# Performance work log

Measured on AMD Instinct MI355X. Metric: run time of the kernel, lower is better.

Reference implementation:

```python
import jax, jax.numpy as jnp
import numpy as np

C = 1024
H = 64
W = 64


def _conv1x1(x, Wt, b):
    # x: [1, Cin, H, W], Wt: [Cout, Cin] -> [1, Cout, H, W]
    return jnp.einsum('oc,bchw->bohw', Wt, x) + b[None, :, None, None]


def setup_inputs() -> dict:
    key = jax.random.key(0)
    ks = jax.random.split(key, 12)
    sc = 1.0 / np.sqrt(C)
    return {
        'x_f': jax.random.normal(ks[0], (1, C, H, W), jnp.float32),
        'x_m': jax.random.normal(ks[1], (1, C, H, W), jnp.float32),
        'x_l': jax.random.normal(ks[2], (1, C, H, W), jnp.float32),
        'Wq': jax.random.normal(ks[3], (C // 2, C), jnp.float32) * sc,
        'bq': jax.random.normal(ks[4], (C // 2,), jnp.float32) * sc,
        'Wk1': jax.random.normal(ks[5], (C // 2, C), jnp.float32) * sc,
        'bk1': jax.random.normal(ks[6], (C // 2,), jnp.float32) * sc,
        'Wk2': jax.random.normal(ks[7], (C // 2, C), jnp.float32) * sc,
        'bk2': jax.random.normal(ks[8], (C // 2,), jnp.float32) * sc,
        'Wv': jax.random.normal(ks[9], (C, C), jnp.float32) * sc,
        'bv': jax.random.normal(ks[10], (C,), jnp.float32) * sc,
        'gamma': jax.random.normal(ks[11], (1,), jnp.float32),
    }


def reference(x_f, x_m, x_l, Wq, bq, Wk1, bk1, Wk2, bk2, Wv, bv, gamma):
    c = x_f.shape[1]
    h, w = x_f.shape[2], x_f.shape[3]
    # torch .view(1, C, -1) on a [1, C/2, H, W] tensor: row-major reshape to [C, H*W/2]
    q = _conv1x1(x_m, Wq, bq).reshape(c, -1).T      # [HW/2, C]
    kf = _conv1x1(x_f, Wk1, bk1).reshape(c, -1)     # [C, HW/2]
    kl = _conv1x1(x_l, Wk2, bk2).reshape(c, -1)     # [C, HW/2]
    att_f = jax.nn.softmax(kf @ q, axis=-1)         # [C, C]
    att_l = jax.nn.softmax(kl @ q, axis=-1)         # [C, C]
    v = _conv1x1(x_m, Wv, bv).reshape(c, -1)        # [C, HW]
    out = att_f @ v + att_l @ v                     # [C, HW]
    out = out.reshape(1, c, h, w)
    return gamma * out + (x_l + x_f) / 2
```

## Files before the change

### kernel.cpp

```cpp
#include <hip/hip_runtime.h>
#include <math.h>


typedef __attribute__((ext_vector_type(8))) short    bf16x8;
typedef __attribute__((ext_vector_type(4))) float    f32x4;

__device__ __forceinline__ unsigned short f2bf(float x) {
    unsigned u = __float_as_uint(x);
    u += 0x7FFFu + ((u >> 16) & 1u);
    return (unsigned short)(u >> 16);
}
__device__ __forceinline__ float bf2f(unsigned short h) {
    return __uint_as_float(((unsigned)h) << 16);
}
__device__ __forceinline__ void split2(float x, unsigned short& h, unsigned short& l) {
    h = f2bf(x);
    l = f2bf(x - bf2f(h));
}

__device__ __forceinline__ size_t swz(int m, int k, int kpan) {
    return ((size_t)((m >> 4) * kpan + (k >> 5))) * 512
         + (size_t)((((k >> 3) & 3) * 16 + (m & 15)) * 8 + (k & 7));
}

__device__ __forceinline__ void gld16(const unsigned short* g, unsigned short* l) {
    __builtin_amdgcn_global_load_lds(
        (const __attribute__((address_space(1))) unsigned int*)g,
        (__attribute__((address_space(3))) unsigned int*)l,
        16, 0, 0);
}

__global__ __launch_bounds__(256) void weights_split_k(
    const float* __restrict__ Wq, const float* __restrict__ Wk1,
    const float* __restrict__ Wk2, const float* __restrict__ Wv,
    unsigned short* __restrict__ Wqh, unsigned short* __restrict__ Wql,
    unsigned short* __restrict__ Wk1h, unsigned short* __restrict__ Wk1l,
    unsigned short* __restrict__ Wk2h, unsigned short* __restrict__ Wk2l,
    unsigned short* __restrict__ Wvh, unsigned short* __restrict__ Wvl)
{
    const int gi = blockIdx.x;
    const float* src; unsigned short *H, *L; int base;
    if (gi < 512)       { src = Wq;  H = Wqh;  L = Wql;  base = gi; }
    else if (gi < 1024) { src = Wk1; H = Wk1h; L = Wk1l; base = gi - 512; }
    else if (gi < 1536) { src = Wk2; H = Wk2h; L = Wk2l; base = gi - 1024; }
    else                { src = Wv;  H = Wvh;  L = Wvl;  base = gi - 1536; }
    const size_t i = (size_t)base * 1024 + threadIdx.x * 4;
    const int m = (int)(i >> 10);
    const int k = (int)(i & 1023);
    const float4 v = *(const float4*)(src + i);
    ushort4 h, l;
    split2(v.x, h.x, l.x); split2(v.y, h.y, l.y);
    split2(v.z, h.z, l.z); split2(v.w, h.w, l.w);
    const size_t o = swz(m, k, 32);
    *(ushort4*)(H + o) = h;
    *(ushort4*)(L + o) = l;
}

__global__ __launch_bounds__(256) void transpose3_k(
    const float* __restrict__ x0, const float* __restrict__ x1,
    const float* __restrict__ x2,
    unsigned short* __restrict__ t0h, unsigned short* __restrict__ t0l,
    unsigned short* __restrict__ t1h, unsigned short* __restrict__ t1l,
    unsigned short* __restrict__ t2h, unsigned short* __restrict__ t2l)
{
    const float* X; unsigned short *Th, *Tl;
    if (blockIdx.z == 0)      { X = x0; Th = t0h; Tl = t0l; }
    else if (blockIdx.z == 1) { X = x1; Th = t1h; Tl = t1l; }
    else                      { X = x2; Th = t2h; Tl = t2l; }

    __shared__ float t[32 * 33];
    const int tid = threadIdx.x;
    const int c0 = blockIdx.y * 32;
    const int p0 = blockIdx.x * 32;

    const int cl = tid >> 3;
    const int p4 = (tid & 7) * 4;
    const float4 v = *(const float4*)(X + (size_t)(c0 + cl) * 4096 + p0 + p4);
    t[(p4 + 0) * 33 + cl] = v.x;
    t[(p4 + 1) * 33 + cl] = v.y;
    t[(p4 + 2) * 33 + cl] = v.z;
    t[(p4 + 3) * 33 + cl] = v.w;
    __syncthreads();

    const int pl = tid >> 3;
    const int c4 = (tid & 7) * 4;
    ushort4 h, l;
    split2(t[pl * 33 + c4 + 0], h.x, l.x);
    split2(t[pl * 33 + c4 + 1], h.y, l.y);
    split2(t[pl * 33 + c4 + 2], h.z, l.z);
    split2(t[pl * 33 + c4 + 3], h.w, l.w);
    const size_t o = (size_t)(p0 + pl) * 1024 + c0 + c4;
    *(ushort4*)(Th + o) = h;
    *(ushort4*)(Tl + o) = l;
}

__global__ __launch_bounds__(256) void transpose1_k(
    const float* __restrict__ X,
    unsigned short* __restrict__ Th, unsigned short* __restrict__ Tl)
{
    __shared__ float t[32 * 33];
    const int tid = threadIdx.x;
    const int c0 = blockIdx.y * 32;
    const int p0 = blockIdx.x * 32;

    const int cl = tid >> 3;
    const int p4 = (tid & 7) * 4;
    const float4 v = *(const float4*)(X + (size_t)(c0 + cl) * 4096 + p0 + p4);
    t[(p4 + 0) * 33 + cl] = v.x;
    t[(p4 + 1) * 33 + cl] = v.y;
    t[(p4 + 2) * 33 + cl] = v.z;
    t[(p4 + 3) * 33 + cl] = v.w;
    __syncthreads();

    const int pl = tid >> 3;
    const int c4 = (tid & 7) * 4;
    ushort4 h, l;
    split2(t[pl * 33 + c4 + 0], h.x, l.x);
    split2(t[pl * 33 + c4 + 1], h.y, l.y);
    split2(t[pl * 33 + c4 + 2], h.z, l.z);
    split2(t[pl * 33 + c4 + 3], h.w, l.w);
    const size_t o = (size_t)(p0 + pl) * 1024 + c0 + c4;
    *(ushort4*)(Th + o) = h;
    *(ushort4*)(Tl + o) = l;
}

template<int TERMS>
__device__ __forceinline__ void gemm_core(
    const unsigned short* __restrict__ Ah, const unsigned short* __restrict__ Al,
    const unsigned short* __restrict__ Bh, const unsigned short* __restrict__ Bl,
    int ldkB, int kpanA, int kbeg, int kend, int m0, int n0,
    unsigned short* Bs_h, unsigned short* Bs_l,
    f32x4 (&acc)[4][4])
{
    const int tid  = threadIdx.x;
    const int lane = tid & 63;
    const int wv   = tid >> 6;
    const int wm   = (wv >> 1) * 64;
    const int wn   = (wv & 1) * 64;
    const int lr   = lane & 15;
    const int quad = lane >> 4;

    const unsigned short* gsrc = (wv < 2) ? Bh : Bl;
    unsigned short* ldst = (wv < 2) ? Bs_h : Bs_l;
    const int tt0  = (wv & 1) * 4;
    const int lrow = lane >> 2;
    const int gseg = ((lane & 3) - ((lane >> 3) & 3)) & 3;
    const unsigned short* gp[4];
#pragma unroll
    for (int u = 0; u < 4; ++u)
        gp[u] = gsrc + (size_t)(n0 + (tt0 + u) * 16 + lrow) * ldkB + kbeg + gseg * 8;

    const int pk0 = kbeg >> 5;
    const unsigned short* ap[4];
    const unsigned short* apl[4];
#pragma unroll
    for (int i = 0; i < 4; ++i) {
        const size_t off = ((size_t)(((m0 + wm) >> 4) + i) * kpanA + pk0) * 512
                         + (size_t)lane * 8;
        ap[i] = Ah + off;
        apl[i] = (TERMS == 3) ? (Al + off) : nullptr;
    }

    const int rdseg = (quad + (lr >> 1)) & 3;

#pragma unroll
    for (int u = 0; u < 4; ++u) {
        gld16(gp[u], ldst + (tt0 + u) * 512);
        gp[u] += 32;
    }

    int buf = 0;
    for (int k0 = kbeg; k0 < kend; k0 += 32) {
        __syncthreads();

        bf16x8 afh[4], afl[4];
#pragma unroll
        for (int i = 0; i < 4; ++i) {
            afh[i] = *(const bf16x8*)ap[i];  ap[i] += 512;
            if (TERMS == 3) { afl[i] = *(const bf16x8*)apl[i]; apl[i] += 512; }
        }
        if (k0 + 32 < kend) {
#pragma unroll
            for (int u = 0; u < 4; ++u) {
                gld16(gp[u], ldst + (buf ^ 1) * 4096 + (tt0 + u) * 512);
                gp[u] += 32;
            }
        }
        bf16x8 bfh[4], bfl[4];
#pragma unroll
        for (int j = 0; j < 4; ++j) {
            const int rb = buf * 4096 + (wn + j * 16 + lr) * 32 + rdseg * 8;
            bfh[j] = *(const bf16x8*)(Bs_h + rb);
            bfl[j] = *(const bf16x8*)(Bs_l + rb);
        }
#pragma unroll
        for (int i = 0; i < 4; ++i)
#pragma unroll
            for (int j = 0; j < 4; ++j) {
                acc[i][j] = __builtin_amdgcn_mfma_f32_16x16x32_bf16(afh[i], bfh[j], acc[i][j], 0, 0, 0);
                acc[i][j] = __builtin_amdgcn_mfma_f32_16x16x32_bf16(afh[i], bfl[j], acc[i][j], 0, 0, 0);
                if (TERMS == 3)
                    acc[i][j] = __builtin_amdgcn_mfma_f32_16x16x32_bf16(afl[i], bfh[j], acc[i][j], 0, 0, 0);
            }
        buf ^= 1;
    }
}

#define GEMM_PROLOGUE()                                                 \
    __shared__ __align__(16) unsigned short Bs_h[2 * 128 * 32];         \
    __shared__ __align__(16) unsigned short Bs_l[2 * 128 * 32];         \
    f32x4 acc[4][4];                                                    \
    _Pragma("unroll") for (int i = 0; i < 4; ++i)                       \
    _Pragma("unroll") for (int j = 0; j < 4; ++j)                       \
    _Pragma("unroll") for (int r = 0; r < 4; ++r) acc[i][j][r] = 0.f;   \
    const int lane = threadIdx.x & 63;                                  \
    const int wv   = threadIdx.x >> 6;                                  \
    const int wm   = (wv >> 1) * 64;                                    \
    const int wn   = (wv & 1) * 64;                                     \
    const int lr   = lane & 15;                                         \
    const int quad = lane >> 4;                                         \
    (void)lane; (void)wv;

__global__ __launch_bounds__(256) void conv_all_k(
    const unsigned short* __restrict__ Wqh, const unsigned short* __restrict__ Wql,
    const unsigned short* __restrict__ Wk1h, const unsigned short* __restrict__ Wk1l,
    const unsigned short* __restrict__ Wk2h, const unsigned short* __restrict__ Wk2l,
    const unsigned short* __restrict__ Wvh, const unsigned short* __restrict__ Wvl,
    const unsigned short* __restrict__ xmTh, const unsigned short* __restrict__ xmTl,
    const unsigned short* __restrict__ xfTh, const unsigned short* __restrict__ xfTl,
    const unsigned short* __restrict__ xlTh, const unsigned short* __restrict__ xlTl,
    const float* __restrict__ bq, const float* __restrict__ bk1,
    const float* __restrict__ bk2, const float* __restrict__ bv,
    unsigned short* __restrict__ Qh, unsigned short* __restrict__ Ql,
    unsigned short* __restrict__ Kfh, unsigned short* __restrict__ Kfl,
    unsigned short* __restrict__ Klh, unsigned short* __restrict__ Kll,
    float* __restrict__ V)
{
    GEMM_PROLOGUE();
    const int mt = blockIdx.y;
    const unsigned short *Ah, *Al, *Bh, *Bl;
    const float* bias;
    unsigned short *Ch = nullptr, *Cl = nullptr;
    float* Cv = nullptr;
    int mloc, mode;
    if (mt < 4) {
        Ah = Wqh;  Al = Wql;  Bh = xmTh; Bl = xmTl; bias = bq;
        Ch = Qh;   Cl = Ql;   mloc = mt * 128;        mode = 0;
    } else if (mt < 8) {
        Ah = Wk1h; Al = Wk1l; Bh = xfTh; Bl = xfTl; bias = bk1;
        Ch = Kfh;  Cl = Kfl;  mloc = (mt - 4) * 128;  mode = 1;
    } else if (mt < 12) {
        Ah = Wk2h; Al = Wk2l; Bh = xlTh; Bl = xlTl; bias = bk2;
        Ch = Klh;  Cl = Kll;  mloc = (mt - 8) * 128;  mode = 1;
    } else {
        Ah = Wvh;  Al = Wvl;  Bh = xmTh; Bl = xmTl; bias = bv;
        Cv = V;    mloc = (mt - 12) * 128;            mode = 2;
    }
    const int n0 = blockIdx.x * 128;

    gemm_core<3>(Ah, Al, Bh, Bl, 1024, 32, 0, 1024, mloc, n0, Bs_h, Bs_l, acc);

#pragma unroll
    for (int i = 0; i < 4; ++i) {
        const int mb = mloc + wm + i * 16 + quad * 4;
#pragma unroll
        for (int j = 0; j < 4; ++j) {
            const int nn = n0 + wn + j * 16 + lr;
#pragma unroll
            for (int r = 0; r < 4; ++r) {
                const float v = acc[i][j][r] + bias[mb + r];
                if (mode == 2) {
                    Cv[(size_t)(mb + r) * 4096 + nn] = v;
                } else if (mode == 0) {
                    unsigned short h, l;
                    split2(v, h, l);
                    const size_t idx = (size_t)(mb + r) * 4096 + nn;
                    Ch[idx] = h;
                    Cl[idx] = l;
                } else {
                    const int m2 = ((mb + r) << 1) | (nn >> 11);
                    const int k2 = nn & 2047;
                    const size_t o = swz(m2, k2, 64);
                    unsigned short h, l;
                    split2(v, h, l);
                    Ch[o] = h;
                    Cl[o] = l;
                }
            }
        }
    }
}

__global__ __launch_bounds__(256) void logits_fused_k(
    const unsigned short* __restrict__ Kfh, const unsigned short* __restrict__ Kfl,
    const unsigned short* __restrict__ Klh, const unsigned short* __restrict__ Kll,
    const unsigned short* __restrict__ Qh, const unsigned short* __restrict__ Ql,
    float* __restrict__ Sfp, float* __restrict__ Slp)
{
    GEMM_PROLOGUE();
    const int which = blockIdx.z >> 2;
    const int slice = blockIdx.z & 3;
    const unsigned short* Ah = which ? Klh : Kfh;
    const unsigned short* Al = which ? Kll : Kfl;
    float* out = (which ? Slp : Sfp) + (size_t)slice * 1024 * 1024;
    const int m0 = blockIdx.y * 128;
    const int n0 = blockIdx.x * 128;

    gemm_core<3>(Ah, Al, Qh, Ql, 2048, 64, slice * 512, slice * 512 + 512, m0, n0,
                 Bs_h, Bs_l, acc);

#pragma unroll
    for (int i = 0; i < 4; ++i) {
        const int mb = m0 + wm + i * 16 + quad * 4;
#pragma unroll
        for (int j = 0; j < 4; ++j) {
            const int nn = n0 + wn + j * 16 + lr;
#pragma unroll
            for (int r = 0; r < 4; ++r)
                out[(size_t)(mb + r) * 1024 + nn] = acc[i][j][r];
        }
    }
}

__global__ __launch_bounds__(256) void gemm_final_k(
    const unsigned short* __restrict__ Amh,
    const unsigned short* __restrict__ VTh, const unsigned short* __restrict__ VTl,
    float* __restrict__ out,
    const float* __restrict__ xf, const float* __restrict__ xl,
    const float* __restrict__ gamma)
{
    GEMM_PROLOGUE();
    const int m0 = blockIdx.y * 128;
    const int n0 = blockIdx.x * 128;

    gemm_core<2>(Amh, nullptr, VTh, VTl, 1024, 32, 0, 1024, m0, n0, Bs_h, Bs_l, acc);

    const float g = gamma[0];
#pragma unroll
    for (int i = 0; i < 4; ++i) {
        const int mb = m0 + wm + i * 16 + quad * 4;
#pragma unroll
        for (int j = 0; j < 4; ++j) {
            const int nn = n0 + wn + j * 16 + lr;
#pragma unroll
            for (int r = 0; r < 4; ++r) {
                const size_t idx = (size_t)(mb + r) * 4096 + nn;
                out[idx] = g * acc[i][j][r] + 0.5f * (xf[idx] + xl[idx]);
            }
        }
    }
}

__global__ __launch_bounds__(256) void softmax_add4_k(
    const float* __restrict__ Sfp, const float* __restrict__ Slp,
    unsigned short* __restrict__ Ah)
{
    const int row = blockIdx.x;
    const int tid = threadIdx.x;
    __shared__ float red[8];
    const size_t base = (size_t)row * 1024 + tid * 4;
    const size_t SL = (size_t)1024 * 1024;

    float4 vf = *(const float4*)(Sfp + base);
    float4 vl = *(const float4*)(Slp + base);
#pragma unroll
    for (int s = 1; s < 4; ++s) {
        const float4 a = *(const float4*)(Sfp + s * SL + base);
        const float4 b = *(const float4*)(Slp + s * SL + base);
        vf.x += a.x; vf.y += a.y; vf.z += a.z; vf.w += a.w;
        vl.x += b.x; vl.y += b.y; vl.z += b.z; vl.w += b.w;
    }

    float mf = fmaxf(fmaxf(vf.x, vf.y), fmaxf(vf.z, vf.w));
    float ml = fmaxf(fmaxf(vl.x, vl.y), fmaxf(vl.z, vl.w));
#pragma unroll
    for (int off = 32; off; off >>= 1) {
        mf = fmaxf(mf, __shfl_down(mf, off, 64));
        ml = fmaxf(ml, __shfl_down(ml, off, 64));
    }
    const int wave = tid >> 6;
    if ((tid & 63) == 0) { red[wave] = mf; red[4 + wave] = ml; }
    __syncthreads();
    mf = fmaxf(fmaxf(red[0], red[1]), fmaxf(red[2], red[3]));
    ml = fmaxf(fmaxf(red[4], red[5]), fmaxf(red[6], red[7]));
    __syncthreads();

    const float4 ef = make_float4(expf(vf.x - mf), expf(vf.y - mf),
                                  expf(vf.z - mf), expf(vf.w - mf));
    const float4 el = make_float4(expf(vl.x - ml), expf(vl.y - ml),
                                  expf(vl.z - ml), expf(vl.w - ml));
    float sf = ef.x + ef.y + ef.z + ef.w;
    float sl = el.x + el.y + el.z + el.w;
#pragma unroll
    for (int off = 32; off; off >>= 1) {
        sf += __shfl_down(sf, off, 64);
        sl += __shfl_down(sl, off, 64);
    }
    if ((tid & 63) == 0) { red[wave] = sf; red[4 + wave] = sl; }
    __syncthreads();
    sf = red[0] + red[1] + red[2] + red[3];
    sl = red[4] + red[5] + red[6] + red[7];

    const float rf = 1.f / sf, rl = 1.f / sl;
    ushort4 h;
    h.x = f2bf(ef.x * rf + el.x * rl);
    h.y = f2bf(ef.y * rf + el.y * rl);
    h.z = f2bf(ef.z * rf + el.z * rl);
    h.w = f2bf(ef.w * rf + el.w * rl);
    const size_t o = swz(row, tid * 4, 32);
    *(ushort4*)(Ah + o) = h;
}

__global__ void noop_k(float* p) { if (threadIdx.x == 1024) p[0] = 0.f; }

extern "C" void kernel_launch(void* const* d_in, const int* in_sizes, int n_in,
                              void* d_out, int out_size, void* d_ws, size_t ws_size,
                              hipStream_t stream) {
    (void)in_sizes; (void)n_in; (void)out_size;
    const float* xf  = (const float*)d_in[0];
    const float* xm  = (const float*)d_in[1];
    const float* xl  = (const float*)d_in[2];
    const float* Wq  = (const float*)d_in[3];
    const float* bq  = (const float*)d_in[4];
    const float* Wk1 = (const float*)d_in[5];
    const float* bk1 = (const float*)d_in[6];
    const float* Wk2 = (const float*)d_in[7];
    const float* bk2 = (const float*)d_in[8];
    const float* Wv  = (const float*)d_in[9];
    const float* bv  = (const float*)d_in[10];
    const float* gamma = (const float*)d_in[11];
    float* out = (float*)d_out;

    const size_t MB = 1024 * 1024;
    if (ws_size < 98 * MB) {
        noop_k<<<dim3(1), dim3(64), 0, stream>>>((float*)d_ws);
        return;
    }

    char* p = (char*)d_ws;
    unsigned short* xmT_h = (unsigned short*)(p + 0 * MB);
    unsigned short* xmT_l = (unsigned short*)(p + 8 * MB);
    unsigned short* xfT_h = (unsigned short*)(p + 16 * MB);
    unsigned short* xfT_l = (unsigned short*)(p + 24 * MB);
    unsigned short* xlT_h = (unsigned short*)(p + 32 * MB);
    unsigned short* xlT_l = (unsigned short*)(p + 40 * MB);
    unsigned short* Wq_h  = (unsigned short*)(p + 48 * MB);
    unsigned short* Wq_l  = (unsigned short*)(p + 49 * MB);
    unsigned short* Wk1_h = (unsigned short*)(p + 50 * MB);
    unsigned short* Wk1_l = (unsigned short*)(p + 51 * MB);
    unsigned short* Wk2_h = (unsigned short*)(p + 52 * MB);
    unsigned short* Wk2_l = (unsigned short*)(p + 53 * MB);
    unsigned short* Wv_h  = (unsigned short*)(p + 54 * MB);
    unsigned short* Wv_l  = (unsigned short*)(p + 56 * MB);
    unsigned short* Q_h   = (unsigned short*)(p + 58 * MB);
    unsigned short* Q_l   = (unsigned short*)(p + 62 * MB);
    unsigned short* Kf_h  = (unsigned short*)(p + 66 * MB);
    unsigned short* Kf_l  = (unsigned short*)(p + 70 * MB);
    unsigned short* Kl_h  = (unsigned short*)(p + 74 * MB);
    unsigned short* Kl_l  = (unsigned short*)(p + 78 * MB);
    float*          V     = (float*)(p + 82 * MB);
    float*          Sfp  = (float*)(p + 16 * MB);
    float*          Slp  = (float*)(p + 32 * MB);
    unsigned short* VT_h = xmT_h;
    unsigned short* VT_l = xmT_l;
    unsigned short* Am_h = (unsigned short*)(p + 74 * MB);

    const dim3 blk(256);
    transpose3_k<<<dim3(128, 32, 3), blk, 0, stream>>>(
        xm, xf, xl, xmT_h, xmT_l, xfT_h, xfT_l, xlT_h, xlT_l);
    weights_split_k<<<dim3(2560), blk, 0, stream>>>(
        Wq, Wk1, Wk2, Wv, Wq_h, Wq_l, Wk1_h, Wk1_l, Wk2_h, Wk2_l, Wv_h, Wv_l);
    conv_all_k<<<dim3(32, 20), blk, 0, stream>>>(
        Wq_h, Wq_l, Wk1_h, Wk1_l, Wk2_h, Wk2_l, Wv_h, Wv_l,
        xmT_h, xmT_l, xfT_h, xfT_l, xlT_h, xlT_l,
        bq, bk1, bk2, bv,
        Q_h, Q_l, Kf_h, Kf_l, Kl_h, Kl_l, V);
    logits_fused_k<<<dim3(8, 8, 8), blk, 0, stream>>>(
        Kf_h, Kf_l, Kl_h, Kl_l, Q_h, Q_l, Sfp, Slp);
    transpose1_k<<<dim3(128, 32), blk, 0, stream>>>(V, VT_h, VT_l);
    softmax_add4_k<<<dim3(1024), blk, 0, stream>>>(Sfp, Slp, Am_h);
    gemm_final_k<<<dim3(32, 8), blk, 0, stream>>>(
        Am_h, VT_h, VT_l, out, xf, xl, gamma);
}
```

Baseline: 301.4 us.

## Widen conv and logits GEMM tiles to 128x256, prefetch A fragments, swizzle block order

The shared GEMM core is templated on the number of N sub-tiles, and the conv and logits kernels now use 128x256 output tiles instead of 128x128, so each A fragment feeds more MFMAs and the grids shrink to 320 and 256 blocks. The K loop is unrolled by two with register double-buffering of the A fragments, loading the next step's A while computing the current one. Block indices are remapped with an XCD-style interleave to improve L2 locality across chiplets. The larger accumulator array raises register pressure (launch_bounds(256,2)), and fewer blocks may leave some CUs idle.

Result: no change. 297.8 us (-1.2%).

```diff
diff --git a/kernel.cpp b/kernel.cpp
--- a/kernel.cpp
+++ b/kernel.cpp
@@ -124,104 +124,114 @@
     *(ushort4*)(Tl + o) = l;
 }
 
-template<int TERMS>
+template<int TERMS, int NJ>
 __device__ __forceinline__ void gemm_core(
     const unsigned short* __restrict__ Ah, const unsigned short* __restrict__ Al,
     const unsigned short* __restrict__ Bh, const unsigned short* __restrict__ Bl,
     int ldkB, int kpanA, int kbeg, int kend, int m0, int n0,
     unsigned short* Bs_h, unsigned short* Bs_l,
-    f32x4 (&acc)[4][4])
+    f32x4 (&acc)[4][NJ])
 {
     const int tid  = threadIdx.x;
     const int lane = tid & 63;
     const int wv   = tid >> 6;
     const int wm   = (wv >> 1) * 64;
-    const int wn   = (wv & 1) * 64;
+    const int wn   = (wv & 1) * (16 * NJ);
     const int lr   = lane & 15;
     const int quad = lane >> 4;
+    const int BUFE = 1024 * NJ;
 
     const unsigned short* gsrc = (wv < 2) ? Bh : Bl;
     unsigned short* ldst = (wv < 2) ? Bs_h : Bs_l;
-    const int tt0  = (wv & 1) * 4;
+    const int tt0  = (wv & 1) * NJ;
     const int lrow = lane >> 2;
     const int gseg = ((lane & 3) - ((lane >> 3) & 3)) & 3;
-    const unsigned short* gp[4];
-#pragma unroll
-    for (int u = 0; u < 4; ++u)
-        gp[u] = gsrc + (size_t)(n0 + (tt0 + u) * 16 + lrow) * ldkB + kbeg + gseg * 8;
+    const size_t bstep = (size_t)16 * (size_t)ldkB;
+    const unsigned short* gp0 =
+        gsrc + (size_t)(n0 + tt0 * 16 + lrow) * ldkB + kbeg + gseg * 8;
 
     const int pk0 = kbeg >> 5;
-    const unsigned short* ap[4];
-    const unsigned short* apl[4];
+    const size_t astr  = (size_t)kpanA * 512;
+    const size_t abase = (size_t)((m0 + wm) >> 4) * astr + (size_t)pk0 * 512
+                       + (size_t)lane * 8;
+    const unsigned short* ap0 = Ah + abase;
+    const unsigned short* al0 = (TERMS == 3) ? (Al + abase) : nullptr;
+
+    const int rdseg = (quad + (lr >> 1)) & 3;
+
+#pragma unroll
+    for (int u = 0; u < NJ; ++u)
+        gld16(gp0 + (size_t)u * bstep, ldst + (tt0 + u) * 512);
+
+    bf16x8 cah[4], cal[4], nah[4], nal[4];
 #pragma unroll
     for (int i = 0; i < 4; ++i) {
-        const size_t off = ((size_t)(((m0 + wm) >> 4) + i) * kpanA + pk0) * 512
-                         + (size_t)lane * 8;
-        ap[i] = Ah + off;
-        apl[i] = (TERMS == 3) ? (Al + off) : nullptr;
-    }
-
-    const int rdseg = (quad + (lr >> 1)) & 3;
-
-#pragma unroll
-    for (int u = 0; u < 4; ++u) {
-        gld16(gp[u], ldst + (tt0 + u) * 512);
-        gp[u] += 32;
-    }
-
+        cah[i] = *(const bf16x8*)(ap0 + (size_t)i * astr);
+        if (TERMS == 3) cal[i] = *(const bf16x8*)(al0 + (size_t)i * astr);
+    }
+
+    const int nsteps = (kend - kbeg) >> 5;
     int buf = 0;
-    for (int k0 = kbeg; k0 < kend; k0 += 32) {
-        __syncthreads();
-
-        bf16x8 afh[4], afl[4];
-#pragma unroll
-        for (int i = 0; i < 4; ++i) {
-            afh[i] = *(const bf16x8*)ap[i];  ap[i] += 512;
-            if (TERMS == 3) { afl[i] = *(const bf16x8*)apl[i]; apl[i] += 512; }
-        }
-        if (k0 + 32 < kend) {
-#pragma unroll
-            for (int u = 0; u < 4; ++u) {
-                gld16(gp[u], ldst + (buf ^ 1) * 4096 + (tt0 + u) * 512);
-                gp[u] += 32;
-            }
-        }
-        bf16x8 bfh[4], bfl[4];
-#pragma unroll
-        for (int j = 0; j < 4; ++j) {
-            const int rb = buf * 4096 + (wn + j * 16 + lr) * 32 + rdseg * 8;
-            bfh[j] = *(const bf16x8*)(Bs_h + rb);
-            bfl[j] = *(const bf16x8*)(Bs_l + rb);
-        }
-#pragma unroll
-        for (int i = 0; i < 4; ++i)
-#pragma unroll
-            for (int j = 0; j < 4; ++j) {
-                acc[i][j] = __builtin_amdgcn_mfma_f32_16x16x32_bf16(afh[i], bfh[j], acc[i][j], 0, 0, 0);
-                acc[i][j] = __builtin_amdgcn_mfma_f32_16x16x32_bf16(afh[i], bfl[j], acc[i][j], 0, 0, 0);
-                if (TERMS == 3)
-                    acc[i][j] = __builtin_amdgcn_mfma_f32_16x16x32_bf16(afl[i], bfh[j], acc[i][j], 0, 0, 0);
-            }
-        buf ^= 1;
-    }
-}
-
-#define GEMM_PROLOGUE()                                                 \
-    __shared__ __align__(16) unsigned short Bs_h[2 * 128 * 32];         \
-    __shared__ __align__(16) unsigned short Bs_l[2 * 128 * 32];         \
-    f32x4 acc[4][4];                                                    \
+
+#define GSTEP(S, CH, CL, NH, NL)                                              \
+    {                                                                         \
+        __syncthreads();                                                      \
+        if ((S) + 1 < nsteps) {                                               \
+            const size_t aoff = (size_t)((S) + 1) * 512;                      \
+            _Pragma("unroll")                                                 \
+            for (int i = 0; i < 4; ++i) {                                     \
+                NH[i] = *(const bf16x8*)(ap0 + (size_t)i * astr + aoff);      \
+                if (TERMS == 3)                                               \
+                    NL[i] = *(const bf16x8*)(al0 + (size_t)i * astr + aoff);  \
+            }                                                                 \
+            const size_t goff = (size_t)((S) + 1) * 32;                      \
+            unsigned short* dst = ldst + (buf ^ 1) * BUFE;                    \
+            _Pragma("unroll")                                                 \
+            for (int u = 0; u < NJ; ++u)                                      \
+                gld16(gp0 + (size_t)u * bstep + goff, dst + (tt0 + u) * 512); \
+        }                                                                     \
+        const int rbase = buf * BUFE + (wn + lr) * 32 + rdseg * 8;            \
+        _Pragma("unroll")                                                     \
+        for (int j = 0; j < NJ; ++j) {                                        \
+            const bf16x8 bh = *(const bf16x8*)(Bs_h + rbase + j * 512);       \
+            const bf16x8 bl = *(const bf16x8*)(Bs_l + rbase + j * 512);       \
+            _Pragma("unroll")                                                 \
+            for (int i = 0; i < 4; ++i) {                                     \
+                acc[i][j] = __builtin_amdgcn_mfma_f32_16x16x32_bf16(          \
+                    CH[i], bh, acc[i][j], 0, 0, 0);                           \
+                acc[i][j] = __builtin_amdgcn_mfma_f32_16x16x32_bf16(          \
+                    CH[i], bl, acc[i][j], 0, 0, 0);                           \
+                if (TERMS == 3)                                               \
+                    acc[i][j] = __builtin_amdgcn_mfma_f32_16x16x32_bf16(      \
+                        CL[i], bh, acc[i][j], 0, 0, 0);                       \
+            }                                                                 \
+        }                                                                     \
+        buf ^= 1;                                                             \
+    }
+
+    for (int s = 0; s < nsteps; s += 2) {
+        GSTEP(s,     cah, cal, nah, nal);
+        GSTEP(s + 1, nah, nal, cah, cal);
+    }
+#undef GSTEP
+}
+
+#define GEMM_PROLOGUE(NJ_)                                              \
+    __shared__ __align__(16) unsigned short Bs_h[2 * 1024 * (NJ_)];     \
+    __shared__ __align__(16) unsigned short Bs_l[2 * 1024 * (NJ_)];     \
+    f32x4 acc[4][(NJ_)];                                                \
     _Pragma("unroll") for (int i = 0; i < 4; ++i)                       \
-    _Pragma("unroll") for (int j = 0; j < 4; ++j)                       \
+    _Pragma("unroll") for (int j = 0; j < (NJ_); ++j)                   \
     _Pragma("unroll") for (int r = 0; r < 4; ++r) acc[i][j][r] = 0.f;   \
     const int lane = threadIdx.x & 63;                                  \
     const int wv   = threadIdx.x >> 6;                                  \
     const int wm   = (wv >> 1) * 64;                                    \
-    const int wn   = (wv & 1) * 64;                                     \
+    const int wn   = (wv & 1) * (16 * (NJ_));                           \
     const int lr   = lane & 15;                                         \
     const int quad = lane >> 4;                                         \
-    (void)lane; (void)wv;
-
-__global__ __launch_bounds__(256) void conv_all_k(
+    (void)lane; (void)wv; (void)wm; (void)wn;
+
+__global__ __launch_bounds__(256, 2) void conv_all_k(
     const unsigned short* __restrict__ Wqh, const unsigned short* __restrict__ Wql,
     const unsigned short* __restrict__ Wk1h, const unsigned short* __restrict__ Wk1l,
     const unsigned short* __restrict__ Wk2h, const unsigned short* __restrict__ Wk2l,
@@ -236,8 +246,12 @@
     unsigned short* __restrict__ Klh, unsigned short* __restrict__ Kll,
     float* __restrict__ V)
 {
-    GEMM_PROLOGUE();
-    const int mt = blockIdx.y;
+    GEMM_PROLOGUE(8);
+    const int lid = blockIdx.y * 16 + blockIdx.x;
+    const int wg  = (lid & 7) * 40 + (lid >> 3);
+    const int mt  = wg >> 4;
+    const int n0  = (wg & 15) * 256;
+
     const unsigned short *Ah, *Al, *Bh, *Bl;
     const float* bias;
     unsigned short *Ch = nullptr, *Cl = nullptr;
@@ -256,15 +270,14 @@
         Ah = Wvh;  Al = Wvl;  Bh = xmTh; Bl = xmTl; bias = bv;
         Cv = V;    mloc = (mt - 12) * 128;            mode = 2;
     }
-    const int n0 = blockIdx.x * 128;
-
-    gemm_core<3>(Ah, Al, Bh, Bl, 1024, 32, 0, 1024, mloc, n0, Bs_h, Bs_l, acc);
+
+    gemm_core<3, 8>(Ah, Al, Bh, Bl, 1024, 32, 0, 1024, mloc, n0, Bs_h, Bs_l, acc);
 
 #pragma unroll
     for (int i = 0; i < 4; ++i) {
         const int mb = mloc + wm + i * 16 + quad * 4;
 #pragma unroll
-        for (int j = 0; j < 4; ++j) {
+        for (int j = 0; j < 8; ++j) {
             const int nn = n0 + wn + j * 16 + lr;
 #pragma unroll
             for (int r = 0; r < 4; ++r) {
@@ -291,29 +304,35 @@
     }
 }
 
-__global__ __launch_bounds__(256) void logits_fused_k(
+__global__ __launch_bounds__(256, 2) void logits_fused_k(
     const unsigned short* __restrict__ Kfh, const unsigned short* __restrict__ Kfl,
     const unsigned short* __restrict__ Klh, const unsigned short* __restrict__ Kll,
     const unsigned short* __restrict__ Qh, const unsigned short* __restrict__ Ql,
     float* __restrict__ Sfp, float* __restrict__ Slp)
 {
-    GEMM_PROLOGUE();
-    const int which = blockIdx.z >> 2;
-    const int slice = blockIdx.z & 3;
+    GEMM_PROLOGUE(8);
+    const int lid = (blockIdx.z * 8 + blockIdx.y) * 4 + blockIdx.x;
+    const int wg  = (lid & 7) * 32 + (lid >> 3);
+    const int bx  = wg & 3;
+    const int by  = (wg >> 2) & 7;
+    const int bz  = wg >> 5;
+
+    const int which = bz >> 2;
+    const int slice = bz & 3;
     const unsigned short* Ah = which ? Klh : Kfh;
     const unsigned short* Al = which ? Kll : Kfl;
     float* out = (which ? Slp : Sfp) + (size_t)slice * 1024 * 1024;
-    const int m0 = blockIdx.y * 128;
-    const int n0 = blockIdx.x * 128;
-
-    gemm_core<3>(Ah, Al, Qh, Ql, 2048, 64, slice * 512, slice * 512 + 512, m0, n0,
-                 Bs_h, Bs_l, acc);
+    const int m0 = by * 128;
+    const int n0 = bx * 256;
+
+    gemm_core<3, 8>(Ah, Al, Qh, Ql, 2048, 64, slice * 512, slice * 512 + 512,
+                    m0, n0, Bs_h, Bs_l, acc);
 
 #pragma unroll
     for (int i = 0; i < 4; ++i) {
         const int mb = m0 + wm + i * 16 + quad * 4;
 #pragma unroll
-        for (int j = 0; j < 4; ++j) {
+        for (int j = 0; j < 8; ++j) {
             const int nn = n0 + wn + j * 16 + lr;
 #pragma unroll
             for (int r = 0; r < 4; ++r)
@@ -329,11 +348,12 @@
     const float* __restrict__ xf, const float* __restrict__ xl,
     const float* __restrict__ gamma)
 {
-    GEMM_PROLOGUE();
+    GEMM_PROLOGUE(4);
     const int m0 = blockIdx.y * 128;
     const int n0 = blockIdx.x * 128;
 
-    gemm_core<2>(Amh, nullptr, VTh, VTl, 1024, 32, 0, 1024, m0, n0, Bs_h, Bs_l, acc);
+    gemm_core<2, 4>(Amh, nullptr, VTh, VTl, 1024, 32, 0, 1024, m0, n0,
+                    Bs_h, Bs_l, acc);
 
     const float g = gamma[0];
 #pragma unroll
@@ -470,12 +490,12 @@
         xm, xf, xl, xmT_h, xmT_l, xfT_h, xfT_l, xlT_h, xlT_l);
     weights_split_k<<<dim3(2560), blk, 0, stream>>>(
         Wq, Wk1, Wk2, Wv, Wq_h, Wq_l, Wk1_h, Wk1_l, Wk2_h, Wk2_l, Wv_h, Wv_l);
-    conv_all_k<<<dim3(32, 20), blk, 0, stream>>>(
+    conv_all_k<<<dim3(16, 20), blk, 0, stream>>>(
         Wq_h, Wq_l, Wk1_h, Wk1_l, Wk2_h, Wk2_l, Wv_h, Wv_l,
         xmT_h, xmT_l, xfT_h, xfT_l, xlT_h, xlT_l,
         bq, bk1, bk2, bv,
         Q_h, Q_l, Kf_h, Kf_l, Kl_h, Kl_l, V);
-    logits_fused_k<<<dim3(8, 8, 8), blk, 0, stream>>>(
+    logits_fused_k<<<dim3(4, 8, 8), blk, 0, stream>>>(
         Kf_h, Kf_l, Kl_h, Kl_l, Q_h, Q_l, Sfp, Slp);
     transpose1_k<<<dim3(128, 32), blk, 0, stream>>>(V, VT_h, VT_l);
     softmax_add4_k<<<dim3(1024), blk, 0, stream>>>(Sfp, Slp, Am_h);
```
